# Optimization experiments

Hardware: AMD Instinct MI355X
Metric: run time of the kernel (lower is better)

## Reference

```python
import jax, jax.numpy as jnp
import numpy as np

N = 100000
E = 1600000
IN_C = 128
HID = 32
H1 = 4
OUT_C = 32
H2 = 1
NEG_SLOPE = 0.2


def setup_inputs() -> dict:
    key = jax.random.key(0)
    ks = jax.random.split(key, 12)
    g = 0.1  # glorot-ish scale
    return {
        "x": jax.random.normal(ks[0], (N, IN_C), jnp.float32),
        "edge_index": jax.random.randint(ks[1], (2, E), 0, N, jnp.int64),
        "W1": jax.random.normal(ks[2], (IN_C, H1 * HID), jnp.float32) * g,
        "att_src1": jax.random.normal(ks[3], (H1, HID), jnp.float32) * g,
        "att_dst1": jax.random.normal(ks[4], (H1, HID), jnp.float32) * g,
        "b1": jnp.zeros((H1 * HID,), jnp.float32),
        "W2": jax.random.normal(ks[5], (H1 * HID, H2 * OUT_C), jnp.float32) * g,
        "att_src2": jax.random.normal(ks[6], (H2, OUT_C), jnp.float32) * g,
        "att_dst2": jax.random.normal(ks[7], (H2, OUT_C), jnp.float32) * g,
        "b2": jnp.zeros((H2 * OUT_C,), jnp.float32),
    }


def gat_conv(x, src, dst, W, att_src, att_dst, bias, heads, ch):
    n = x.shape[0]
    h = (x @ W).reshape(n, heads, ch)                      # [N,H,C]
    a_src = jnp.sum(h * att_src, axis=-1)                  # [N,H]
    a_dst = jnp.sum(h * att_dst, axis=-1)                  # [N,H]
    e = jax.nn.leaky_relu(a_src[src] + a_dst[dst], NEG_SLOPE)  # [E,H]
    # segment softmax over destination neighborhoods
    m = jax.ops.segment_max(e, dst, num_segments=n)        # [N,H]
    ex = jnp.exp(e - m[dst])
    denom = jax.ops.segment_sum(ex, dst, num_segments=n)   # [N,H]
    alpha = ex / (denom[dst] + 1e-16)                      # [E,H]
    msg = h[src] * alpha[:, :, None]                       # [E,H,C]
    out = jax.ops.segment_sum(msg, dst, num_segments=n)    # [N,H,C]
    return out.reshape(n, heads * ch) + bias


def reference(x, edge_index, W1, att_src1, att_dst1, b1, W2, att_src2, att_dst2, b2):
    # PyG GATConv add_self_loops=True
    loops = jnp.arange(N, dtype=edge_index.dtype)
    src = jnp.concatenate([edge_index[0], loops])
    dst = jnp.concatenate([edge_index[1], loops])
    # dropout is a no-op at inference
    h = gat_conv(x, src, dst, W1, att_src1, att_dst1, b1, H1, HID)
    h = jax.nn.relu(h)
    out = gat_conv(h, src, dst, W2, att_src2, att_dst2, b2, H2, OUT_C)
    return out
```

## Files before the change

### kernel.cpp

```cpp
#include <hip/hip_runtime.h>
#include <hip/hip_bf16.h>


#define NSLOPE 0.2f
#define GSTRIDE 136
#define NB_MAX 400
#define CHUNK 4096
#define CAP 5632

typedef __attribute__((ext_vector_type(8))) short short8;
typedef __attribute__((ext_vector_type(4))) float floatx4;

__device__ __forceinline__ float leaky(float v) { return v > 0.f ? v : NSLOPE * v; }

__device__ __forceinline__ unsigned short f2bf(float f) {
  __hip_bfloat16 b = __float2bfloat16(f);
  return *reinterpret_cast<unsigned short*>(&b);
}
__device__ __forceinline__ float bf2f(unsigned int u) {
  return __uint_as_float(u << 16);
}
__device__ __forceinline__ unsigned int pack2(float a, float b) {
  return (unsigned int)f2bf(a) | ((unsigned int)f2bf(b) << 16);
}

__global__ __launch_bounds__(256, 2) void fused1_kernel(
    const float* __restrict__ x, const float* __restrict__ W,
    const float* __restrict__ atts, const float* __restrict__ attd,
    unsigned short* __restrict__ h, float* __restrict__ asrc, float* __restrict__ adst,
    int n, int g1blocks,
    const int* __restrict__ ei, int* __restrict__ bincur,
    unsigned int* __restrict__ staging, int E, int ET, int nb) {
  __shared__ __align__(16) unsigned char smem[70656];
  const int tid = threadIdx.x;

  if (blockIdx.x < g1blocks) {
    unsigned short* xs = (unsigned short*)smem;
    unsigned short* wt = (unsigned short*)(smem + 34816);
    float* att_s = (float*)(smem + 69632);
    float* att_d = (float*)(smem + 70144);
    const int row0 = blockIdx.x * 128;

    if (tid < 128) { att_s[tid] = atts[tid]; att_d[tid] = attd[tid]; }

    const float4* w4 = (const float4*)W;
#pragma unroll
    for (int i = 0; i < 16; i++) {
      int idx = tid + i * 256;
      int k = idx >> 5, n0 = (idx & 31) * 4;
      float4 v = w4[idx];
      float vv[4] = {v.x, v.y, v.z, v.w};
#pragma unroll
      for (int jj = 0; jj < 4; jj++) {
        int j = (jj + tid) & 3;
        wt[(n0 + j) * GSTRIDE + k] = f2bf(vv[j]);
      }
    }

    const float4* x4 = (const float4*)x;
#pragma unroll
    for (int i = 0; i < 16; i++) {
      int idx = tid + i * 256;
      int r = idx >> 5, c4 = idx & 31;
      float4 v = make_float4(0.f, 0.f, 0.f, 0.f);
      if (row0 + r < n) v = x4[(size_t)(row0 + r) * 32 + c4];
      unsigned int* p = (unsigned int*)&xs[r * GSTRIDE + c4 * 4];
      p[0] = pack2(v.x, v.y);
      p[1] = pack2(v.z, v.w);
    }
    __syncthreads();

    const int l = tid & 63;
    const int w = tid >> 6;
    const int mrow = l & 15;
    const int q = l >> 4;
    floatx4 acc[2][8];
#pragma unroll
    for (int mt = 0; mt < 2; mt++)
#pragma unroll
      for (int nt = 0; nt < 8; nt++) acc[mt][nt] = (floatx4){0.f, 0.f, 0.f, 0.f};

#pragma unroll
    for (int ks = 0; ks < 4; ks++) {
      const int k0 = ks * 32 + q * 8;
      short8 a0 = *(const short8*)&xs[(w * 32 + mrow) * GSTRIDE + k0];
      short8 a1 = *(const short8*)&xs[(w * 32 + 16 + mrow) * GSTRIDE + k0];
#pragma unroll
      for (int nt = 0; nt < 8; nt++) {
        short8 b = *(const short8*)&wt[(nt * 16 + mrow) * GSTRIDE + k0];
        acc[0][nt] = __builtin_amdgcn_mfma_f32_16x16x32_bf16(a0, b, acc[0][nt], 0, 0, 0);
        acc[1][nt] = __builtin_amdgcn_mfma_f32_16x16x32_bf16(a1, b, acc[1][nt], 0, 0, 0);
      }
    }
    __syncthreads();

#pragma unroll
    for (int mt = 0; mt < 2; mt++)
#pragma unroll
      for (int nt = 0; nt < 8; nt++)
#pragma unroll
        for (int i = 0; i < 4; i++) {
          int r = w * 32 + mt * 16 + q * 4 + i;
          xs[r * GSTRIDE + nt * 16 + mrow] = f2bf(acc[mt][nt][i]);
        }
    __syncthreads();

#pragma unroll
    for (int i = 0; i < 8; i++) {
      int idx = tid + i * 256;
      int r = idx >> 4, c8 = (idx & 15) * 8;
      if (row0 + r < n) {
        unsigned int* p = (unsigned int*)&xs[r * GSTRIDE + c8];
        uint4 v = make_uint4(p[0], p[1], p[2], p[3]);
        *(uint4*)(h + (size_t)(row0 + r) * 128 + c8) = v;
      }
    }

#pragma unroll
    for (int rr = 0; rr < 2; rr++) {
      int row = (tid >> 2) + rr * 64;
      int head = tid & 3;
      float ss = 0.f, sd = 0.f;
#pragma unroll
      for (int c = 0; c < 32; c++) {
        int cr = (c + tid) & 31;
        float hv = bf2f(xs[row * GSTRIDE + head * 32 + cr]);
        ss += hv * att_s[head * 32 + cr];
        sd += hv * att_d[head * 32 + cr];
      }
      if (row0 + row < n) {
        asrc[(size_t)(row0 + row) * 4 + head] = ss;
        adst[(size_t)(row0 + row) * 4 + head] = sd;
      }
    }
  } else {
    int* hist  = (int*)smem;
    int* run   = (int*)(smem + 1600);
    int* rbase = (int*)(smem + 3200);
    const int base = (blockIdx.x - g1blocks) * CHUNK;
    for (int i = tid; i < nb; i += 256) { hist[i] = 0; run[i] = 0; }
    __syncthreads();
    int se[16], de[16];
#pragma unroll
    for (int j = 0; j < 16; j++) {
      int idx = base + j * 256 + tid;
      if (idx < ET) {
        if (idx < E) { se[j] = ei[idx]; de[j] = ei[E + idx]; }
        else         { se[j] = de[j] = idx - E; }
        atomicAdd(&hist[de[j] >> 8], 1);
      } else de[j] = -1;
    }
    __syncthreads();
    for (int i = tid; i < nb; i += 256)
      rbase[i] = hist[i] ? (i * CAP + atomicAdd(&bincur[i], hist[i])) : 0;
    __syncthreads();
#pragma unroll
    for (int j = 0; j < 16; j++) {
      if (de[j] >= 0) {
        int b = de[j] >> 8;
        int ofs = atomicAdd(&run[b], 1);
        staging[(size_t)rbase[b] + ofs] =
            (unsigned)se[j] | ((unsigned)(de[j] & 255) << 17);
      }
    }
  }
}

__global__ __launch_bounds__(1024) void binB_kernel(const unsigned int* __restrict__ staging,
                                                    const int* __restrict__ bincur,
                                                    int* __restrict__ rowbeg,
                                                    int* __restrict__ rowend,
                                                    int* __restrict__ bucket, int n) {
  __shared__ int cnt[256];
  __shared__ int cur[256];
  const int b = blockIdx.x;
  const int t = threadIdx.x;
  const int d0 = b << 8;
  const int nd = min(256, n - d0);
  const int base = b * CAP;
  const int rcnt = bincur[b];
  if (t < 256) cnt[t] = 0;
  __syncthreads();
  for (int j = t; j < rcnt; j += 1024) {
    unsigned int r = staging[(size_t)base + j];
    atomicAdd(&cnt[r >> 17], 1);
  }
  __syncthreads();
  int v = 0;
  if (t < 256) { v = cnt[t]; cur[t] = v; }
  __syncthreads();
  for (int off = 1; off < 256; off <<= 1) {
    int add = (t < 256 && t >= off) ? cur[t - off] : 0;
    __syncthreads();
    if (t < 256) cur[t] += add;
    __syncthreads();
  }
  if (t < 256) {
    int start = base + cur[t] - v;
    if (t < nd) { rowbeg[d0 + t] = start; rowend[d0 + t] = start + v; }
    cur[t] = start;
  }
  __syncthreads();
  for (int j = t; j < rcnt; j += 1024) {
    unsigned int r = staging[(size_t)base + j];
    int pos = atomicAdd(&cur[r >> 17], 1);
    bucket[pos] = (int)(r & 0x1FFFFu);
  }
}

__global__ __launch_bounds__(256) void g1_kernel(const int* __restrict__ rowbeg,
                                                 const int* __restrict__ rowend,
                                                 const int* __restrict__ bucket,
                                                 const float* __restrict__ asrc,
                                                 const float* __restrict__ adst,
                                                 const unsigned int* __restrict__ h,
                                                 const float* __restrict__ b1,
                                                 unsigned short* __restrict__ x2,
                                                 int n) {
  const int lane = threadIdx.x & 63;
  const int g = lane >> 3;
  const int l8 = lane & 7;
  const int head = l8 >> 1;
  const int d = blockIdx.x * 4 + (threadIdx.x >> 6);
  if (d >= n) return;
  const float ad = adst[(size_t)d * 4 + head];
  const int beg = rowbeg[d], end = rowend[d];
  float num[16];
#pragma unroll
  for (int j = 0; j < 16; j++) num[j] = 0.f;
  float den = 0.f;

  int i = beg + g;
  if (i < end) {
    int s = bucket[i];
    for (;;) {
      float a = asrc[(size_t)s * 4 + head];
      const uint4* hp = (const uint4*)(h + (size_t)s * 64 + l8 * 8);
      uint4 h0 = hp[0];
      uint4 h1v = hp[1];
      int i2 = i + 8;
      int s2 = (i2 < end) ? bucket[i2] : 0;
      float w = __expf(leaky(a + ad));
      den += w;
      num[0]  += w * bf2f(h0.x & 0xffffu);  num[1]  += w * bf2f(h0.x >> 16);
      num[2]  += w * bf2f(h0.y & 0xffffu);  num[3]  += w * bf2f(h0.y >> 16);
      num[4]  += w * bf2f(h0.z & 0xffffu);  num[5]  += w * bf2f(h0.z >> 16);
      num[6]  += w * bf2f(h0.w & 0xffffu);  num[7]  += w * bf2f(h0.w >> 16);
      num[8]  += w * bf2f(h1v.x & 0xffffu); num[9]  += w * bf2f(h1v.x >> 16);
      num[10] += w * bf2f(h1v.y & 0xffffu); num[11] += w * bf2f(h1v.y >> 16);
      num[12] += w * bf2f(h1v.z & 0xffffu); num[13] += w * bf2f(h1v.z >> 16);
      num[14] += w * bf2f(h1v.w & 0xffffu); num[15] += w * bf2f(h1v.w >> 16);
      if (i2 >= end) break;
      i = i2; s = s2;
    }
  }
#pragma unroll
  for (int j = 0; j < 16; j++) {
    num[j] += __shfl_xor(num[j], 8, 64);
    num[j] += __shfl_xor(num[j], 16, 64);
    num[j] += __shfl_xor(num[j], 32, 64);
  }
  den += __shfl_xor(den, 8, 64);
  den += __shfl_xor(den, 16, 64);
  den += __shfl_xor(den, 32, 64);
  if (g == 0) {
    float inv = 1.f / (den + 1e-16f);
    const float4* b14 = (const float4*)b1;
    float4 bb[4] = {b14[l8 * 4], b14[l8 * 4 + 1], b14[l8 * 4 + 2], b14[l8 * 4 + 3]};
    const float* bbf = (const float*)bb;
    unsigned short* p = x2 + (size_t)d * 128 + l8 * 16;
    uint4 o0, o1;
    o0.x = pack2(fmaxf(num[0] * inv + bbf[0], 0.f),  fmaxf(num[1] * inv + bbf[1], 0.f));
    o0.y = pack2(fmaxf(num[2] * inv + bbf[2], 0.f),  fmaxf(num[3] * inv + bbf[3], 0.f));
    o0.z = pack2(fmaxf(num[4] * inv + bbf[4], 0.f),  fmaxf(num[5] * inv + bbf[5], 0.f));
    o0.w = pack2(fmaxf(num[6] * inv + bbf[6], 0.f),  fmaxf(num[7] * inv + bbf[7], 0.f));
    o1.x = pack2(fmaxf(num[8] * inv + bbf[8], 0.f),  fmaxf(num[9] * inv + bbf[9], 0.f));
    o1.y = pack2(fmaxf(num[10] * inv + bbf[10], 0.f), fmaxf(num[11] * inv + bbf[11], 0.f));
    o1.z = pack2(fmaxf(num[12] * inv + bbf[12], 0.f), fmaxf(num[13] * inv + bbf[13], 0.f));
    o1.w = pack2(fmaxf(num[14] * inv + bbf[14], 0.f), fmaxf(num[15] * inv + bbf[15], 0.f));
    *(uint4*)p = o0;
    *(uint4*)(p + 8) = o1;
  }
}

__global__ __launch_bounds__(256, 2) void gemm2_kernel(const unsigned short* __restrict__ x2,
                                                       const float* __restrict__ W,
                                                       const float* __restrict__ atts,
                                                       const float* __restrict__ attd,
                                                       unsigned short* __restrict__ h2,
                                                       float* __restrict__ asrc,
                                                       float* __restrict__ adst, int n) {
  __shared__ __align__(16) unsigned short xs[128 * GSTRIDE];
  __shared__ __align__(16) unsigned short wt[32 * GSTRIDE];
  __shared__ __align__(16) unsigned short hs[128 * 36];
  __shared__ float att_s[32], att_d[32];
  const int tid = threadIdx.x;
  const int row0 = blockIdx.x * 128;

  if (tid < 32) { att_s[tid] = atts[tid]; att_d[tid] = attd[tid]; }

  const float4* w4 = (const float4*)W;
#pragma unroll
  for (int i = 0; i < 4; i++) {
    int idx = tid + i * 256;
    int k = idx >> 3, n0 = (idx & 7) * 4;
    float4 v = w4[idx];
    float vv[4] = {v.x, v.y, v.z, v.w};
#pragma unroll
    for (int jj = 0; jj < 4; jj++) {
      int j = (jj + tid) & 3;
      wt[(n0 + j) * GSTRIDE + k] = f2bf(vv[j]);
    }
  }

  const uint4* a4 = (const uint4*)x2;
#pragma unroll
  for (int i = 0; i < 8; i++) {
    int idx = tid + i * 256;
    int r = idx >> 4, c8 = (idx & 15) * 8;
    uint4 v = make_uint4(0, 0, 0, 0);
    if (row0 + r < n) v = a4[(size_t)(row0 + r) * 16 + (idx & 15)];
    unsigned int* p = (unsigned int*)&xs[r * GSTRIDE + c8];
    p[0] = v.x; p[1] = v.y; p[2] = v.z; p[3] = v.w;
  }
  __syncthreads();

  const int l = tid & 63;
  const int w = tid >> 6;
  const int mrow = l & 15;
  const int q = l >> 4;
  floatx4 acc[2][2];
#pragma unroll
  for (int mt = 0; mt < 2; mt++)
#pragma unroll
    for (int nt = 0; nt < 2; nt++) acc[mt][nt] = (floatx4){0.f, 0.f, 0.f, 0.f};

#pragma unroll
  for (int ks = 0; ks < 4; ks++) {
    const int k0 = ks * 32 + q * 8;
    short8 a0 = *(const short8*)&xs[(w * 32 + mrow) * GSTRIDE + k0];
    short8 a1 = *(const short8*)&xs[(w * 32 + 16 + mrow) * GSTRIDE + k0];
#pragma unroll
    for (int nt = 0; nt < 2; nt++) {
      short8 b = *(const short8*)&wt[(nt * 16 + mrow) * GSTRIDE + k0];
      acc[0][nt] = __builtin_amdgcn_mfma_f32_16x16x32_bf16(a0, b, acc[0][nt], 0, 0, 0);
      acc[1][nt] = __builtin_amdgcn_mfma_f32_16x16x32_bf16(a1, b, acc[1][nt], 0, 0, 0);
    }
  }

#pragma unroll
  for (int mt = 0; mt < 2; mt++)
#pragma unroll
    for (int nt = 0; nt < 2; nt++)
#pragma unroll
      for (int i = 0; i < 4; i++) {
        int r = w * 32 + mt * 16 + q * 4 + i;
        hs[r * 36 + nt * 16 + mrow] = f2bf(acc[mt][nt][i]);
      }
  __syncthreads();

#pragma unroll
  for (int i = 0; i < 4; i++) {
    int idx = tid + i * 256;
    int r = idx >> 3, c4 = (idx & 7) * 4;
    if (row0 + r < n) {
      unsigned int* p = (unsigned int*)&hs[r * 36 + c4];
      *(uint2*)(h2 + (size_t)(row0 + r) * 32 + c4) = make_uint2(p[0], p[1]);
    }
  }

  if (tid < 128) {
    int row = tid;
    float ss = 0.f, sd = 0.f;
#pragma unroll
    for (int c = 0; c < 32; c++) {
      int cr = (c + tid) & 31;
      float hv = bf2f(hs[row * 36 + cr]);
      ss += hv * att_s[cr];
      sd += hv * att_d[cr];
    }
    if (row0 + row < n) { asrc[row0 + row] = ss; adst[row0 + row] = sd; }
  }
}

__global__ __launch_bounds__(256) void g2_kernel(const int* __restrict__ rowbeg,
                                                 const int* __restrict__ rowend,
                                                 const int* __restrict__ bucket,
                                                 const float* __restrict__ asrc,
                                                 const float* __restrict__ adst,
                                                 const unsigned int* __restrict__ h2,
                                                 const float* __restrict__ b2,
                                                 float* __restrict__ out, int n) {
  const int lane = threadIdx.x & 63;
  const int g = lane >> 3;
  const int l8 = lane & 7;
  const int d = blockIdx.x * 4 + (threadIdx.x >> 6);
  if (d >= n) return;
  const float ad = adst[d];
  const int beg = rowbeg[d], end = rowend[d];
  float num[4];
#pragma unroll
  for (int j = 0; j < 4; j++) num[j] = 0.f;
  float den = 0.f;

  int i = beg + g;
  if (i < end) {
    int s = bucket[i];
    for (;;) {
      float a = asrc[s];
      uint2 hv = *(const uint2*)(h2 + (size_t)s * 16 + l8 * 2);
      int i2 = i + 8;
      int s2 = (i2 < end) ? bucket[i2] : 0;
      float w = __expf(leaky(a + ad));
      den += w;
      num[0] += w * bf2f(hv.x & 0xffffu); num[1] += w * bf2f(hv.x >> 16);
      num[2] += w * bf2f(hv.y & 0xffffu); num[3] += w * bf2f(hv.y >> 16);
      if (i2 >= end) break;
      i = i2; s = s2;
    }
  }
#pragma unroll
  for (int j = 0; j < 4; j++) {
    num[j] += __shfl_xor(num[j], 8, 64);
    num[j] += __shfl_xor(num[j], 16, 64);
    num[j] += __shfl_xor(num[j], 32, 64);
  }
  den += __shfl_xor(den, 8, 64);
  den += __shfl_xor(den, 16, 64);
  den += __shfl_xor(den, 32, 64);
  if (g == 0) {
    float inv = 1.f / (den + 1e-16f);
    float4 bb = ((const float4*)b2)[l8];
    *(float4*)(out + (size_t)d * 32 + l8 * 4) =
        make_float4(num[0] * inv + bb.x, num[1] * inv + bb.y,
                    num[2] * inv + bb.z, num[3] * inv + bb.w);
  }
}

extern "C" void kernel_launch(void* const* d_in, const int* in_sizes, int n_in,
                              void* d_out, int out_size, void* d_ws, size_t ws_size,
                              hipStream_t stream) {
  const float* x = (const float*)d_in[0];
  const int* ei = (const int*)d_in[1];
  const float* W1 = (const float*)d_in[2];
  const float* atts1 = (const float*)d_in[3];
  const float* attd1 = (const float*)d_in[4];
  const float* b1 = (const float*)d_in[5];
  const float* W2 = (const float*)d_in[6];
  const float* atts2 = (const float*)d_in[7];
  const float* attd2 = (const float*)d_in[8];
  const float* b2 = (const float*)d_in[9];
  float* out = (float*)d_out;

  const int N = in_sizes[0] / 128;
  const int E = in_sizes[1] / 2;
  const int ET = E + N;
  const int NB = (N + 255) >> 8;
  const int NCH = (ET + CHUNK - 1) / CHUNK;
  const int G1B = (N + 127) / 128;

  float* wsf = (float*)d_ws;
  float* asrc1 = wsf;
  float* adst1 = asrc1 + (size_t)N * 4;
  float* asrc2 = adst1 + (size_t)N * 4;
  float* adst2 = asrc2 + (size_t)N;
  unsigned short* x2 = (unsigned short*)(adst2 + (size_t)N);
  unsigned short* h1 = x2 + (size_t)N * 128;
  unsigned short* h2 = h1;
  int* rowbeg = (int*)(h1 + (size_t)N * 128);
  int* rowend = rowbeg + N;
  int* bucket = rowend + N;
  unsigned int* staging = (unsigned int*)(bucket + (size_t)NB * CAP);
  int* bincur = (int*)(staging + (size_t)NB * CAP);

  hipMemsetAsync(bincur, 0, NB * sizeof(int), stream);
  fused1_kernel<<<G1B + NCH, 256, 0, stream>>>(x, W1, atts1, attd1, h1, asrc1, adst1,
                                               N, G1B, ei, bincur, staging, E, ET, NB);
  binB_kernel<<<NB, 1024, 0, stream>>>(staging, bincur, rowbeg, rowend, bucket, N);
  g1_kernel<<<(N + 3) / 4, 256, 0, stream>>>(rowbeg, rowend, bucket, asrc1, adst1,
                                             (const unsigned int*)h1, b1, x2, N);
  gemm2_kernel<<<(N + 127) / 128, 256, 0, stream>>>(x2, W2, atts2, attd2,
                                                    h2, asrc2, adst2, N);
  g2_kernel<<<(N + 3) / 4, 256, 0, stream>>>(rowbeg, rowend, bucket, asrc2, adst2,
                                             (const unsigned int*)h2, b2, out, N);
}
```

Baseline: 283.4 us.

## Fuse layer-2 linear transform and attention logits into layer-1 aggregation kernel

The separate MFMA gemm2 kernel is removed. Each wave in g1 now multiplies its aggregated, ReLU'd 128-wide row by W2 from LDS with FP32 FMAs and shuffle reductions. The same wave writes h2 and the layer-2 source/destination attention scalars. This avoids writing and re-reading the bf16 x2 intermediate and saves a launch. In exchange, every block reloads the full 16 KB W2 into shared memory and does the GEMM on vector ALUs, which adds L2 traffic and LDS pressure that may reduce occupancy.

```diff
diff --git a/kernel.cpp b/kernel.cpp
--- a/kernel.cpp
+++ b/kernel.cpp
@@ -215,13 +215,30 @@
                                                  const float* __restrict__ adst,
                                                  const unsigned int* __restrict__ h,
                                                  const float* __restrict__ b1,
-                                                 unsigned short* __restrict__ x2,
+                                                 const float* __restrict__ W2,
+                                                 const float* __restrict__ atts2,
+                                                 const float* __restrict__ attd2,
+                                                 unsigned short* __restrict__ h2,
+                                                 float* __restrict__ asrc2,
+                                                 float* __restrict__ adst2,
                                                  int n) {
-  const int lane = threadIdx.x & 63;
+  __shared__ __align__(16) float W2ld[128 * 32];
+  __shared__ __align__(16) float xvld[4][128];
+  const int tid = threadIdx.x;
+  {
+    const float4* w4 = (const float4*)W2;
+    float4* wl = (float4*)W2ld;
+#pragma unroll
+    for (int i = 0; i < 4; i++) wl[tid + i * 256] = w4[tid + i * 256];
+  }
+  __syncthreads();
+
+  const int lane = tid & 63;
   const int g = lane >> 3;
   const int l8 = lane & 7;
   const int head = l8 >> 1;
-  const int d = blockIdx.x * 4 + (threadIdx.x >> 6);
+  const int wv = tid >> 6;
+  const int d = blockIdx.x * 4 + wv;
   if (d >= n) return;
   const float ad = adst[(size_t)d * 4 + head];
   const int beg = rowbeg[d], end = rowend[d];
@@ -263,124 +280,43 @@
   den += __shfl_xor(den, 8, 64);
   den += __shfl_xor(den, 16, 64);
   den += __shfl_xor(den, 32, 64);
+  const float inv = 1.f / (den + 1e-16f);
   if (g == 0) {
-    float inv = 1.f / (den + 1e-16f);
     const float4* b14 = (const float4*)b1;
-    float4 bb[4] = {b14[l8 * 4], b14[l8 * 4 + 1], b14[l8 * 4 + 2], b14[l8 * 4 + 3]};
-    const float* bbf = (const float*)bb;
-    unsigned short* p = x2 + (size_t)d * 128 + l8 * 16;
-    uint4 o0, o1;
-    o0.x = pack2(fmaxf(num[0] * inv + bbf[0], 0.f),  fmaxf(num[1] * inv + bbf[1], 0.f));
-    o0.y = pack2(fmaxf(num[2] * inv + bbf[2], 0.f),  fmaxf(num[3] * inv + bbf[3], 0.f));
-    o0.z = pack2(fmaxf(num[4] * inv + bbf[4], 0.f),  fmaxf(num[5] * inv + bbf[5], 0.f));
-    o0.w = pack2(fmaxf(num[6] * inv + bbf[6], 0.f),  fmaxf(num[7] * inv + bbf[7], 0.f));
-    o1.x = pack2(fmaxf(num[8] * inv + bbf[8], 0.f),  fmaxf(num[9] * inv + bbf[9], 0.f));
-    o1.y = pack2(fmaxf(num[10] * inv + bbf[10], 0.f), fmaxf(num[11] * inv + bbf[11], 0.f));
-    o1.z = pack2(fmaxf(num[12] * inv + bbf[12], 0.f), fmaxf(num[13] * inv + bbf[13], 0.f));
-    o1.w = pack2(fmaxf(num[14] * inv + bbf[14], 0.f), fmaxf(num[15] * inv + bbf[15], 0.f));
-    *(uint4*)p = o0;
-    *(uint4*)(p + 8) = o1;
-  }
-}
-
-__global__ __launch_bounds__(256, 2) void gemm2_kernel(const unsigned short* __restrict__ x2,
-                                                       const float* __restrict__ W,
-                                                       const float* __restrict__ atts,
-                                                       const float* __restrict__ attd,
-                                                       unsigned short* __restrict__ h2,
-                                                       float* __restrict__ asrc,
-                                                       float* __restrict__ adst, int n) {
-  __shared__ __align__(16) unsigned short xs[128 * GSTRIDE];
-  __shared__ __align__(16) unsigned short wt[32 * GSTRIDE];
-  __shared__ __align__(16) unsigned short hs[128 * 36];
-  __shared__ float att_s[32], att_d[32];
-  const int tid = threadIdx.x;
-  const int row0 = blockIdx.x * 128;
-
-  if (tid < 32) { att_s[tid] = atts[tid]; att_d[tid] = attd[tid]; }
-
-  const float4* w4 = (const float4*)W;
-#pragma unroll
-  for (int i = 0; i < 4; i++) {
-    int idx = tid + i * 256;
-    int k = idx >> 3, n0 = (idx & 7) * 4;
-    float4 v = w4[idx];
-    float vv[4] = {v.x, v.y, v.z, v.w};
-#pragma unroll
-    for (int jj = 0; jj < 4; jj++) {
-      int j = (jj + tid) & 3;
-      wt[(n0 + j) * GSTRIDE + k] = f2bf(vv[j]);
-    }
-  }
-
-  const uint4* a4 = (const uint4*)x2;
-#pragma unroll
-  for (int i = 0; i < 8; i++) {
-    int idx = tid + i * 256;
-    int r = idx >> 4, c8 = (idx & 15) * 8;
-    uint4 v = make_uint4(0, 0, 0, 0);
-    if (row0 + r < n) v = a4[(size_t)(row0 + r) * 16 + (idx & 15)];
-    unsigned int* p = (unsigned int*)&xs[r * GSTRIDE + c8];
-    p[0] = v.x; p[1] = v.y; p[2] = v.z; p[3] = v.w;
-  }
-  __syncthreads();
-
-  const int l = tid & 63;
-  const int w = tid >> 6;
-  const int mrow = l & 15;
-  const int q = l >> 4;
-  floatx4 acc[2][2];
-#pragma unroll
-  for (int mt = 0; mt < 2; mt++)
-#pragma unroll
-    for (int nt = 0; nt < 2; nt++) acc[mt][nt] = (floatx4){0.f, 0.f, 0.f, 0.f};
-
-#pragma unroll
-  for (int ks = 0; ks < 4; ks++) {
-    const int k0 = ks * 32 + q * 8;
-    short8 a0 = *(const short8*)&xs[(w * 32 + mrow) * GSTRIDE + k0];
-    short8 a1 = *(const short8*)&xs[(w * 32 + 16 + mrow) * GSTRIDE + k0];
-#pragma unroll
-    for (int nt = 0; nt < 2; nt++) {
-      short8 b = *(const short8*)&wt[(nt * 16 + mrow) * GSTRIDE + k0];
-      acc[0][nt] = __builtin_amdgcn_mfma_f32_16x16x32_bf16(a0, b, acc[0][nt], 0, 0, 0);
-      acc[1][nt] = __builtin_amdgcn_mfma_f32_16x16x32_bf16(a1, b, acc[1][nt], 0, 0, 0);
-    }
-  }
-
-#pragma unroll
-  for (int mt = 0; mt < 2; mt++)
-#pragma unroll
-    for (int nt = 0; nt < 2; nt++)
-#pragma unroll
-      for (int i = 0; i < 4; i++) {
-        int r = w * 32 + mt * 16 + q * 4 + i;
-        hs[r * 36 + nt * 16 + mrow] = f2bf(acc[mt][nt][i]);
-      }
-  __syncthreads();
-
-#pragma unroll
-  for (int i = 0; i < 4; i++) {
-    int idx = tid + i * 256;
-    int r = idx >> 3, c4 = (idx & 7) * 4;
-    if (row0 + r < n) {
-      unsigned int* p = (unsigned int*)&hs[r * 36 + c4];
-      *(uint2*)(h2 + (size_t)(row0 + r) * 32 + c4) = make_uint2(p[0], p[1]);
-    }
-  }
-
-  if (tid < 128) {
-    int row = tid;
-    float ss = 0.f, sd = 0.f;
-#pragma unroll
-    for (int c = 0; c < 32; c++) {
-      int cr = (c + tid) & 31;
-      float hv = bf2f(hs[row * 36 + cr]);
-      ss += hv * att_s[cr];
-      sd += hv * att_d[cr];
-    }
-    if (row0 + row < n) { asrc[row0 + row] = ss; adst[row0 + row] = sd; }
-  }
+    float4* xp = (float4*)&xvld[wv][l8 * 16];
+#pragma unroll
+    for (int k = 0; k < 4; k++) {
+      float4 bb = b14[l8 * 4 + k];
+      xp[k] = make_float4(fmaxf(num[k * 4 + 0] * inv + bb.x, 0.f),
+                          fmaxf(num[k * 4 + 1] * inv + bb.y, 0.f),
+                          fmaxf(num[k * 4 + 2] * inv + bb.z, 0.f),
+                          fmaxf(num[k * 4 + 3] * inv + bb.w, 0.f));
+    }
+  }
+  const int ocq = lane & 7;
+  const int cb = lane >> 3;
+  float p0 = 0.f, p1 = 0.f, p2 = 0.f, p3 = 0.f;
+#pragma unroll
+  for (int cc = 0; cc < 16; cc++) {
+    int c = cb * 16 + cc;
+    float xc = xvld[wv][c];
+    float4 w4 = *(const float4*)&W2ld[c * 32 + ocq * 4];
+    p0 += xc * w4.x; p1 += xc * w4.y; p2 += xc * w4.z; p3 += xc * w4.w;
+  }
+  p0 += __shfl_xor(p0, 8, 64); p0 += __shfl_xor(p0, 16, 64); p0 += __shfl_xor(p0, 32, 64);
+  p1 += __shfl_xor(p1, 8, 64); p1 += __shfl_xor(p1, 16, 64); p1 += __shfl_xor(p1, 32, 64);
+  p2 += __shfl_xor(p2, 8, 64); p2 += __shfl_xor(p2, 16, 64); p2 += __shfl_xor(p2, 32, 64);
+  p3 += __shfl_xor(p3, 8, 64); p3 += __shfl_xor(p3, 16, 64); p3 += __shfl_xor(p3, 32, 64);
+  if (cb == 0) {
+    *(uint2*)(h2 + (size_t)d * 32 + ocq * 4) = make_uint2(pack2(p0, p1), pack2(p2, p3));
+  }
+  float4 as4 = ((const float4*)atts2)[ocq];
+  float4 ad4 = ((const float4*)attd2)[ocq];
+  float s2 = p0 * as4.x + p1 * as4.y + p2 * as4.z + p3 * as4.w;
+  float t2 = p0 * ad4.x + p1 * ad4.y + p2 * ad4.z + p3 * ad4.w;
+  s2 += __shfl_xor(s2, 1, 64); s2 += __shfl_xor(s2, 2, 64); s2 += __shfl_xor(s2, 4, 64);
+  t2 += __shfl_xor(t2, 1, 64); t2 += __shfl_xor(t2, 2, 64); t2 += __shfl_xor(t2, 4, 64);
+  if (lane == 0) { asrc2[d] = s2; adst2[d] = t2; }
 }
 
 __global__ __launch_bounds__(256) void g2_kernel(const int* __restrict__ rowbeg,
@@ -464,10 +400,9 @@
   float* adst1 = asrc1 + (size_t)N * 4;
   float* asrc2 = adst1 + (size_t)N * 4;
   float* adst2 = asrc2 + (size_t)N;
-  unsigned short* x2 = (unsigned short*)(adst2 + (size_t)N);
-  unsigned short* h1 = x2 + (size_t)N * 128;
-  unsigned short* h2 = h1;
-  int* rowbeg = (int*)(h1 + (size_t)N * 128);
+  unsigned short* h1 = (unsigned short*)(adst2 + (size_t)N);
+  unsigned short* h2 = h1 + (size_t)N * 128;
+  int* rowbeg = (int*)(h2 + (size_t)N * 32);
   int* rowend = rowbeg + N;
   int* bucket = rowend + N;
   unsigned int* staging = (unsigned int*)(bucket + (size_t)NB * CAP);
@@ -478,9 +413,8 @@
                                                N, G1B, ei, bincur, staging, E, ET, NB);
   binB_kernel<<<NB, 1024, 0, stream>>>(staging, bincur, rowbeg, rowend, bucket, N);
   g1_kernel<<<(N + 3) / 4, 256, 0, stream>>>(rowbeg, rowend, bucket, asrc1, adst1,
-                                             (const unsigned int*)h1, b1, x2, N);
-  gemm2_kernel<<<(N + 127) / 128, 256, 0, stream>>>(x2, W2, atts2, attd2,
-                                                    h2, asrc2, adst2, N);
+                                             (const unsigned int*)h1, b1,
+                                             W2, atts2, attd2, h2, asrc2, adst2, N);
   g2_kernel<<<(N + 3) / 4, 256, 0, stream>>>(rowbeg, rowend, bucket, asrc2, adst2,
                                              (const unsigned int*)h2, b2, out, N);
 }
```

After: 316.6 us. 11.7% more time.

## Prepack weights to bf16 once and read B fragments from global memory

Applied to the files above, without the earlier changes.

Adds a small prepack kernel that converts W1 and W2 to transposed bf16 once and zeroes the bin counters, replacing the memset. The GEMM kernels then stop converting and transposing the weights into shared memory in every block and load B fragments directly from global memory, which should hit in L2. The smaller LDS footprint allows more blocks per CU, so launch bounds are raised. The cost is one extra kernel launch, plus B fragments now coming from global/L2 rather than LDS.

```diff
diff --git a/kernel.cpp b/kernel.cpp
--- a/kernel.cpp
+++ b/kernel.cpp
@@ -24,38 +24,50 @@
   return (unsigned int)f2bf(a) | ((unsigned int)f2bf(b) << 16);
 }
 
-__global__ __launch_bounds__(256, 2) void fused1_kernel(
-    const float* __restrict__ x, const float* __restrict__ W,
+__global__ __launch_bounds__(256) void prepack_kernel(const float* __restrict__ W1,
+                                                      const float* __restrict__ W2,
+                                                      unsigned short* __restrict__ w1p,
+                                                      unsigned short* __restrict__ w2p,
+                                                      int* __restrict__ bincur, int nb) {
+  const int tid = threadIdx.x;
+  if (blockIdx.x == 0) {
+    for (int i = tid; i < nb; i += 256) bincur[i] = 0;
+    unsigned int* o = (unsigned int*)w2p;
+#pragma unroll
+    for (int i = 0; i < 8; i++) {
+      int idx = tid + i * 256;
+      int nn = idx >> 6, k2 = (idx & 63) * 2;
+      o[idx] = pack2(W2[(size_t)k2 * 32 + nn], W2[(size_t)(k2 + 1) * 32 + nn]);
+    }
+  } else {
+    unsigned int* o = (unsigned int*)w1p;
+    int base = (blockIdx.x - 1) * 1024;
+#pragma unroll
+    for (int i = 0; i < 4; i++) {
+      int idx = base + tid + i * 256;
+      int nn = idx >> 6, k2 = (idx & 63) * 2;
+      o[idx] = pack2(W1[(size_t)k2 * 128 + nn], W1[(size_t)(k2 + 1) * 128 + nn]);
+    }
+  }
+}
+
+__global__ __launch_bounds__(256, 4) void fused1_kernel(
+    const float* __restrict__ x, const unsigned short* __restrict__ w1p,
     const float* __restrict__ atts, const float* __restrict__ attd,
     unsigned short* __restrict__ h, float* __restrict__ asrc, float* __restrict__ adst,
     int n, int g1blocks,
     const int* __restrict__ ei, int* __restrict__ bincur,
     unsigned int* __restrict__ staging, int E, int ET, int nb) {
-  __shared__ __align__(16) unsigned char smem[70656];
+  __shared__ __align__(16) unsigned char smem[35840];
   const int tid = threadIdx.x;
 
   if (blockIdx.x < g1blocks) {
     unsigned short* xs = (unsigned short*)smem;
-    unsigned short* wt = (unsigned short*)(smem + 34816);
-    float* att_s = (float*)(smem + 69632);
-    float* att_d = (float*)(smem + 70144);
+    float* att_s = (float*)(smem + 34816);
+    float* att_d = (float*)(smem + 35328);
     const int row0 = blockIdx.x * 128;
 
     if (tid < 128) { att_s[tid] = atts[tid]; att_d[tid] = attd[tid]; }
-
-    const float4* w4 = (const float4*)W;
-#pragma unroll
-    for (int i = 0; i < 16; i++) {
-      int idx = tid + i * 256;
-      int k = idx >> 5, n0 = (idx & 31) * 4;
-      float4 v = w4[idx];
-      float vv[4] = {v.x, v.y, v.z, v.w};
-#pragma unroll
-      for (int jj = 0; jj < 4; jj++) {
-        int j = (jj + tid) & 3;
-        wt[(n0 + j) * GSTRIDE + k] = f2bf(vv[j]);
-      }
-    }
 
     const float4* x4 = (const float4*)x;
 #pragma unroll
@@ -80,16 +92,20 @@
 #pragma unroll
       for (int nt = 0; nt < 8; nt++) acc[mt][nt] = (floatx4){0.f, 0.f, 0.f, 0.f};
 
+    short8 af[2][4];
 #pragma unroll
     for (int ks = 0; ks < 4; ks++) {
       const int k0 = ks * 32 + q * 8;
-      short8 a0 = *(const short8*)&xs[(w * 32 + mrow) * GSTRIDE + k0];
-      short8 a1 = *(const short8*)&xs[(w * 32 + 16 + mrow) * GSTRIDE + k0];
-#pragma unroll
-      for (int nt = 0; nt < 8; nt++) {
-        short8 b = *(const short8*)&wt[(nt * 16 + mrow) * GSTRIDE + k0];
-        acc[0][nt] = __builtin_amdgcn_mfma_f32_16x16x32_bf16(a0, b, acc[0][nt], 0, 0, 0);
-        acc[1][nt] = __builtin_amdgcn_mfma_f32_16x16x32_bf16(a1, b, acc[1][nt], 0, 0, 0);
+      af[0][ks] = *(const short8*)&xs[(w * 32 + mrow) * GSTRIDE + k0];
+      af[1][ks] = *(const short8*)&xs[(w * 32 + 16 + mrow) * GSTRIDE + k0];
+    }
+#pragma unroll
+    for (int nt = 0; nt < 8; nt++) {
+#pragma unroll
+      for (int ks = 0; ks < 4; ks++) {
+        short8 b = *(const short8*)&w1p[(nt * 16 + mrow) * 128 + ks * 32 + q * 8];
+        acc[0][nt] = __builtin_amdgcn_mfma_f32_16x16x32_bf16(af[0][ks], b, acc[0][nt], 0, 0, 0);
+        acc[1][nt] = __builtin_amdgcn_mfma_f32_16x16x32_bf16(af[1][ks], b, acc[1][nt], 0, 0, 0);
       }
     }
     __syncthreads();
@@ -283,35 +299,20 @@
   }
 }
 
-__global__ __launch_bounds__(256, 2) void gemm2_kernel(const unsigned short* __restrict__ x2,
-                                                       const float* __restrict__ W,
+__global__ __launch_bounds__(256, 3) void gemm2_kernel(const unsigned short* __restrict__ x2,
+                                                       const unsigned short* __restrict__ w2p,
                                                        const float* __restrict__ atts,
                                                        const float* __restrict__ attd,
                                                        unsigned short* __restrict__ h2,
                                                        float* __restrict__ asrc,
                                                        float* __restrict__ adst, int n) {
   __shared__ __align__(16) unsigned short xs[128 * GSTRIDE];
-  __shared__ __align__(16) unsigned short wt[32 * GSTRIDE];
   __shared__ __align__(16) unsigned short hs[128 * 36];
   __shared__ float att_s[32], att_d[32];
   const int tid = threadIdx.x;
   const int row0 = blockIdx.x * 128;
 
   if (tid < 32) { att_s[tid] = atts[tid]; att_d[tid] = attd[tid]; }
-
-  const float4* w4 = (const float4*)W;
-#pragma unroll
-  for (int i = 0; i < 4; i++) {
-    int idx = tid + i * 256;
-    int k = idx >> 3, n0 = (idx & 7) * 4;
-    float4 v = w4[idx];
-    float vv[4] = {v.x, v.y, v.z, v.w};
-#pragma unroll
-    for (int jj = 0; jj < 4; jj++) {
-      int j = (jj + tid) & 3;
-      wt[(n0 + j) * GSTRIDE + k] = f2bf(vv[j]);
-    }
-  }
 
   const uint4* a4 = (const uint4*)x2;
 #pragma unroll
@@ -335,16 +336,20 @@
 #pragma unroll
     for (int nt = 0; nt < 2; nt++) acc[mt][nt] = (floatx4){0.f, 0.f, 0.f, 0.f};
 
+  short8 af[2][4];
 #pragma unroll
   for (int ks = 0; ks < 4; ks++) {
     const int k0 = ks * 32 + q * 8;
-    short8 a0 = *(const short8*)&xs[(w * 32 + mrow) * GSTRIDE + k0];
-    short8 a1 = *(const short8*)&xs[(w * 32 + 16 + mrow) * GSTRIDE + k0];
-#pragma unroll
-    for (int nt = 0; nt < 2; nt++) {
-      short8 b = *(const short8*)&wt[(nt * 16 + mrow) * GSTRIDE + k0];
-      acc[0][nt] = __builtin_amdgcn_mfma_f32_16x16x32_bf16(a0, b, acc[0][nt], 0, 0, 0);
-      acc[1][nt] = __builtin_amdgcn_mfma_f32_16x16x32_bf16(a1, b, acc[1][nt], 0, 0, 0);
+    af[0][ks] = *(const short8*)&xs[(w * 32 + mrow) * GSTRIDE + k0];
+    af[1][ks] = *(const short8*)&xs[(w * 32 + 16 + mrow) * GSTRIDE + k0];
+  }
+#pragma unroll
+  for (int nt = 0; nt < 2; nt++) {
+#pragma unroll
+    for (int ks = 0; ks < 4; ks++) {
+      short8 b = *(const short8*)&w2p[(nt * 16 + mrow) * 128 + ks * 32 + q * 8];
+      acc[0][nt] = __builtin_amdgcn_mfma_f32_16x16x32_bf16(af[0][ks], b, acc[0][nt], 0, 0, 0);
+      acc[1][nt] = __builtin_amdgcn_mfma_f32_16x16x32_bf16(af[1][ks], b, acc[1][nt], 0, 0, 0);
     }
   }
 
@@ -472,14 +477,16 @@
   int* bucket = rowend + N;
   unsigned int* staging = (unsigned int*)(bucket + (size_t)NB * CAP);
   int* bincur = (int*)(staging + (size_t)NB * CAP);
-
-  hipMemsetAsync(bincur, 0, NB * sizeof(int), stream);
-  fused1_kernel<<<G1B + NCH, 256, 0, stream>>>(x, W1, atts1, attd1, h1, asrc1, adst1,
+  unsigned short* w1p = (unsigned short*)(bincur + NB_MAX);
+  unsigned short* w2p = w1p + 16384;
+
+  prepack_kernel<<<9, 256, 0, stream>>>(W1, W2, w1p, w2p, bincur, NB);
+  fused1_kernel<<<G1B + NCH, 256, 0, stream>>>(x, w1p, atts1, attd1, h1, asrc1, adst1,
                                                N, G1B, ei, bincur, staging, E, ET, NB);
   binB_kernel<<<NB, 1024, 0, stream>>>(staging, bincur, rowbeg, rowend, bucket, N);
   g1_kernel<<<(N + 3) / 4, 256, 0, stream>>>(rowbeg, rowend, bucket, asrc1, adst1,
                                              (const unsigned int*)h1, b1, x2, N);
-  gemm2_kernel<<<(N + 127) / 128, 256, 0, stream>>>(x2, W2, atts2, attd2,
+  gemm2_kernel<<<(N + 127) / 128, 256, 0, stream>>>(x2, w2p, atts2, attd2,
                                                     h2, asrc2, adst2, N);
   g2_kernel<<<(N + 3) / 4, 256, 0, stream>>>(rowbeg, rowend, bucket, asrc2, adst2,
                                              (const unsigned int*)h2, b2, out, N);
```

Result: no change. 281.2 us (-0.8%).

## Stream W in 16-column slices to shrink LDS and raise occupancy

Applied to the files above, without the earlier changes.

The first-layer GEMM no longer stages the full transposed 128x128 W matrix in shared memory. It loads one 16-column slice at a time and runs the MFMAs for that slice before loading the next. Each warp's A fragments are preloaded into registers. This cuts the fused kernel's LDS footprint from about 70KB to about 40KB, and launch bounds are raised to allow 4 blocks per CU. The cost is 14 extra block-wide barriers and serialized slice loads. The accumulator array is also indexed by a loop variable that is not forced to unroll, which risks scratch spills.

```diff
diff --git a/kernel.cpp b/kernel.cpp
--- a/kernel.cpp
+++ b/kernel.cpp
@@ -24,38 +24,44 @@
   return (unsigned int)f2bf(a) | ((unsigned int)f2bf(b) << 16);
 }
 
-__global__ __launch_bounds__(256, 2) void fused1_kernel(
+__global__ __launch_bounds__(256, 4) void fused1_kernel(
     const float* __restrict__ x, const float* __restrict__ W,
     const float* __restrict__ atts, const float* __restrict__ attd,
     unsigned short* __restrict__ h, float* __restrict__ asrc, float* __restrict__ adst,
     int n, int g1blocks,
     const int* __restrict__ ei, int* __restrict__ bincur,
     unsigned int* __restrict__ staging, int E, int ET, int nb) {
-  __shared__ __align__(16) unsigned char smem[70656];
+  __shared__ __align__(16) unsigned char smem[40192];
   const int tid = threadIdx.x;
 
   if (blockIdx.x < g1blocks) {
     unsigned short* xs = (unsigned short*)smem;
     unsigned short* wt = (unsigned short*)(smem + 34816);
-    float* att_s = (float*)(smem + 69632);
-    float* att_d = (float*)(smem + 70144);
+    float* att_s = (float*)(smem + 39168);
+    float* att_d = (float*)(smem + 39680);
     const int row0 = blockIdx.x * 128;
 
     if (tid < 128) { att_s[tid] = atts[tid]; att_d[tid] = attd[tid]; }
 
     const float4* w4 = (const float4*)W;
-#pragma unroll
-    for (int i = 0; i < 16; i++) {
-      int idx = tid + i * 256;
-      int k = idx >> 5, n0 = (idx & 31) * 4;
-      float4 v = w4[idx];
-      float vv[4] = {v.x, v.y, v.z, v.w};
-#pragma unroll
-      for (int jj = 0; jj < 4; jj++) {
-        int j = (jj + tid) & 3;
-        wt[(n0 + j) * GSTRIDE + k] = f2bf(vv[j]);
-      }
-    }
+#define STAGE_W_16(p)                                                       \
+    {                                                                       \
+      _Pragma("unroll")                                                     \
+      for (int i = 0; i < 2; i++) {                                         \
+        int idx = tid + i * 256;                           \
+        int k = idx >> 2, c4 = idx & 3;                                     \
+        float4 v = w4[k * 32 + (p) * 4 + c4];                               \
+        float vv[4] = {v.x, v.y, v.z, v.w};                                 \
+        int n0 = c4 * 4;                                                    \
+        _Pragma("unroll")                                                   \
+        for (int jj = 0; jj < 4; jj++) {                                    \
+          int j = (jj + tid) & 3;                                           \
+          wt[(n0 + j) * GSTRIDE + k] = f2bf(vv[j]);                         \
+        }                                                                   \
+      }                                                                     \
+    }
+
+    STAGE_W_16(0)
 
     const float4* x4 = (const float4*)x;
 #pragma unroll
@@ -74,22 +80,36 @@
     const int w = tid >> 6;
     const int mrow = l & 15;
     const int q = l >> 4;
-    floatx4 acc[2][8];
-#pragma unroll
-    for (int mt = 0; mt < 2; mt++)
-#pragma unroll
-      for (int nt = 0; nt < 8; nt++) acc[mt][nt] = (floatx4){0.f, 0.f, 0.f, 0.f};
-
+
+    short8 af[2][4];
 #pragma unroll
     for (int ks = 0; ks < 4; ks++) {
       const int k0 = ks * 32 + q * 8;
-      short8 a0 = *(const short8*)&xs[(w * 32 + mrow) * GSTRIDE + k0];
-      short8 a1 = *(const short8*)&xs[(w * 32 + 16 + mrow) * GSTRIDE + k0];
-#pragma unroll
-      for (int nt = 0; nt < 8; nt++) {
-        short8 b = *(const short8*)&wt[(nt * 16 + mrow) * GSTRIDE + k0];
-        acc[0][nt] = __builtin_amdgcn_mfma_f32_16x16x32_bf16(a0, b, acc[0][nt], 0, 0, 0);
-        acc[1][nt] = __builtin_amdgcn_mfma_f32_16x16x32_bf16(a1, b, acc[1][nt], 0, 0, 0);
+      af[0][ks] = *(const short8*)&xs[(w * 32 + mrow) * GSTRIDE + k0];
+      af[1][ks] = *(const short8*)&xs[(w * 32 + 16 + mrow) * GSTRIDE + k0];
+    }
+
+    floatx4 acc[2][8];
+#pragma unroll
+    for (int mt = 0; mt < 2; mt++)
+#pragma unroll
+      for (int nt = 0; nt < 8; nt++) acc[mt][nt] = (floatx4){0.f, 0.f, 0.f, 0.f};
+
+#pragma unroll
+    for (int ks = 0; ks < 4; ks++) {
+      short8 b = *(const short8*)&wt[mrow * GSTRIDE + ks * 32 + q * 8];
+      acc[0][0] = __builtin_amdgcn_mfma_f32_16x16x32_bf16(af[0][ks], b, acc[0][0], 0, 0, 0);
+      acc[1][0] = __builtin_amdgcn_mfma_f32_16x16x32_bf16(af[1][ks], b, acc[1][0], 0, 0, 0);
+    }
+    for (int p = 1; p < 8; p++) {
+      __syncthreads();
+      STAGE_W_16(p)
+      __syncthreads();
+#pragma unroll
+      for (int ks = 0; ks < 4; ks++) {
+        short8 b = *(const short8*)&wt[mrow * GSTRIDE + ks * 32 + q * 8];
+        acc[0][p] = __builtin_amdgcn_mfma_f32_16x16x32_bf16(af[0][ks], b, acc[0][p], 0, 0, 0);
+        acc[1][p] = __builtin_amdgcn_mfma_f32_16x16x32_bf16(af[1][ks], b, acc[1][p], 0, 0, 0);
       }
     }
     __syncthreads();
```

After: 273.6 us. 3.5% less time.
